# Optimization experiments

Measured on AMD Instinct MI355X. Metric: run time of the kernel, lower is better.

## Reference

```python
import jax, jax.numpy as jnp
import numpy as np

BETA = 0.95
NUM_STEPS = 32


def setup_inputs() -> dict:
    key = jax.random.key(0)
    ks = jax.random.split(key, 6)
    B, IN, D, P = 1024, 512, 256, 8
    total = D * P
    x = jax.random.normal(ks[0], (B, IN), jnp.float32)
    W_proj = jax.random.normal(ks[1], (IN, total), jnp.float32) / np.sqrt(IN)
    b_proj = jnp.zeros((total,), jnp.float32)
    # uniform threshold distribution, sorted: linspace(0.5, 2.0, P)
    thresholds = jnp.linspace(0.5, 2.0, P, dtype=jnp.float32)
    rate_W = jax.random.normal(ks[2], (P, 1), jnp.float32) / np.sqrt(P)
    rate_b = jnp.zeros((1,), jnp.float32)
    conv1_w = jax.random.normal(ks[3], (P // 2, P, 3), jnp.float32) / np.sqrt(P * 3)
    conv1_b = jnp.zeros((P // 2,), jnp.float32)
    conv2_w = jax.random.normal(ks[4], (1, P // 2, 1), jnp.float32) / np.sqrt(P // 2)
    conv2_b = jnp.zeros((1,), jnp.float32)
    fusion = jnp.array([0.6, 0.4], jnp.float32)
    return dict(x=x, W_proj=W_proj, b_proj=b_proj, thresholds=thresholds,
                rate_W=rate_W, rate_b=rate_b, conv1_w=conv1_w, conv1_b=conv1_b,
                conv2_w=conv2_w, conv2_b=conv2_b, fusion=fusion)


def _conv1d(x, w, b):
    # x: [N, C_in, T], w: [C_out, C_in, K] -> [N, C_out, T] (SAME padding)
    y = jax.lax.conv_general_dilated(x, w, window_strides=(1,), padding='SAME',
                                     dimension_numbers=('NCH', 'OIH', 'NCH'))
    return y + b[None, :, None]


def reference(x, W_proj, b_proj, thresholds, rate_W, rate_b,
              conv1_w, conv1_b, conv2_w, conv2_b, fusion):
    B = x.shape[0]
    P = thresholds.shape[0]
    D = W_proj.shape[1] // P
    # constant input current per neuron: [B, D, P]
    I = (x @ W_proj + b_proj).reshape(B, D, P)

    # LIF recurrence (snntorch Leaky, reset_mechanism='subtract'):
    #   reset = H(mem_prev - thr); mem = beta*mem_prev + I - reset*thr; spk = H(mem - thr)
    def step(mem, _):
        reset = (mem > thresholds).astype(mem.dtype)
        mem = BETA * mem + I - reset * thresholds
        spk = (mem > thresholds).astype(mem.dtype)
        return mem, spk

    mem0 = jnp.zeros((B, D, P), x.dtype)
    _, spikes = jax.lax.scan(step, mem0, None, length=NUM_STEPS)  # [T, B, D, P]

    # rate branch
    rates = spikes.mean(axis=0)                        # [B, D, P]
    rate_dec = (rates @ rate_W)[..., 0] + rate_b[0]    # [B, D]

    # temporal branch: [B*D, P, T]
    s = jnp.transpose(spikes, (1, 2, 3, 0)).reshape(B * D, P, NUM_STEPS)
    h = jax.nn.relu(_conv1d(s, conv1_w, conv1_b))
    h = _conv1d(h, conv2_w, conv2_b)                   # [B*D, 1, T]
    temp_dec = h.mean(axis=-1).reshape(B, D)

    fw = jax.nn.softmax(fusion)
    return fw[0] * rate_dec + fw[1] * temp_dec
```

## Files before the change

### kernel.cpp

```cpp
#include <hip/hip_runtime.h>
#include <type_traits>


constexpr int IN_DIM  = 512;
constexpr int D_DIM   = 256;
constexpr int NTOT    = 2048;
constexpr int T_STEPS = 32;

typedef _Float16 f16x8 __attribute__((ext_vector_type(8)));
typedef float    f32x4 __attribute__((ext_vector_type(4)));
typedef ushort   ushort8 __attribute__((ext_vector_type(8)));

#define GLOBAL_AS __attribute__((address_space(1)))
#define LDS_AS    __attribute__((address_space(3)))

__device__ __forceinline__ void split_f16(float v, ushort& h, ushort& l) {
    const _Float16 hf = (_Float16)v;
    const _Float16 lf = (_Float16)((v - (float)hf) * 2048.0f);
    h = __builtin_bit_cast(ushort, hf);
    l = __builtin_bit_cast(ushort, lf);
}

__global__ __launch_bounds__(256)
void popcode_prep(const float* __restrict__ x, const float* __restrict__ Wp,
                  ushort* __restrict__ Ah, ushort* __restrict__ Al,
                  ushort* __restrict__ Bh, ushort* __restrict__ Bl)
{
    __shared__ float tile[64][68];
    const int t = threadIdx.x;
    if (blockIdx.x < 256) {
        const int idx = (blockIdx.x * 256 + t) * 8;
        float v[8];
        *reinterpret_cast<float4*>(v)     = *reinterpret_cast<const float4*>(x + idx);
        *reinterpret_cast<float4*>(v + 4) = *reinterpret_cast<const float4*>(x + idx + 4);
        __align__(16) ushort h[8], l[8];
#pragma unroll
        for (int j = 0; j < 8; ++j) split_f16(v[j], h[j], l[j]);
        *reinterpret_cast<ushort8*>(Ah + idx) = *reinterpret_cast<const ushort8*>(h);
        *reinterpret_cast<ushort8*>(Al + idx) = *reinterpret_cast<const ushort8*>(l);
    } else {
        const int ib = blockIdx.x - 256;
        const int k0 = (ib >> 5) * 64;
        const int c0 = (ib & 31) * 64;
        {
            const int r = t >> 2, cq = (t & 3) * 16;
#pragma unroll
            for (int j = 0; j < 4; ++j)
                *reinterpret_cast<float4*>(&tile[r][cq + j * 4]) =
                    *reinterpret_cast<const float4*>(Wp + (size_t)(k0 + r) * NTOT + c0 + cq + j * 4);
        }
        __syncthreads();
        const int c = t & 63, kq = (t >> 6) * 16;
        __align__(16) ushort h[16], l[16];
#pragma unroll
        for (int j = 0; j < 16; ++j) split_f16(tile[kq + j][c], h[j], l[j]);
        ushort* dh = Bh + (size_t)(c0 + c) * 512 + k0 + kq;
        ushort* dl = Bl + (size_t)(c0 + c) * 512 + k0 + kq;
        *reinterpret_cast<ushort8*>(dh)     = *reinterpret_cast<const ushort8*>(h);
        *reinterpret_cast<ushort8*>(dh + 8) = *reinterpret_cast<const ushort8*>(h + 8);
        *reinterpret_cast<ushort8*>(dl)     = *reinterpret_cast<const ushort8*>(l);
        *reinterpret_cast<ushort8*>(dl + 8) = *reinterpret_cast<const ushort8*>(l + 8);
    }
}

__global__ __launch_bounds__(256, 2)
void popcode_mfma(const ushort* __restrict__ Ah_g, const ushort* __restrict__ Al_g,
                  const ushort* __restrict__ Bh_g, const ushort* __restrict__ Bl_g,
                  float* __restrict__ Iout)
{
    __shared__ __align__(16) ushort Lds[2][4][64][32];

    const int tid  = threadIdx.x;
    const int w    = tid >> 6;
    const int lane = tid & 63;
    const int b0   = blockIdx.x * 64;
    const int c0   = blockIdx.y * 64;

    const ushort* gbase = (w == 0) ? Ah_g : (w == 1) ? Al_g : (w == 2) ? Bh_g : Bl_g;
    const int     t0    = (w < 2) ? b0 : c0;
    const int     srow  = lane >> 2;
    const int     schk  = (lane & 3) * 8;

    const int wr = (w >> 1) * 32;
    const int wc = (w & 1) * 32;
    const int lr = lane & 15;
    const int lg = lane >> 4;

    const f32x4 zero = {0.f, 0.f, 0.f, 0.f};
    f32x4 acch[2][2] = {{zero, zero}, {zero, zero}};
    f32x4 accl[2][2] = {{zero, zero}, {zero, zero}};

    LDS_AS char* lds0 = (LDS_AS char*)&Lds[0][0][0][0];

    auto stage = [&](int buf, int kt) {
        const int koff = kt * 32 + schk;
#pragma unroll
        for (int i = 0; i < 4; ++i) {
            const ushort* src = gbase + (size_t)(t0 + srow + 16 * i) * 512 + koff;
            const int loff = __builtin_amdgcn_readfirstlane(buf * 16384 + w * 4096 + i * 1024);
            __builtin_amdgcn_global_load_lds((const GLOBAL_AS uint*)src,
                                             (LDS_AS uint*)(lds0 + loff), 16, 0, 0);
        }
    };

    auto compute = [&](int buf) {
        f16x8 ah[2], al[2], bh[2], bl[2];
#pragma unroll
        for (int m = 0; m < 2; ++m) {
            const int row = wr + m * 16 + lr;
            ah[m] = *(const f16x8*)&Lds[buf][0][row][lg * 8];
            al[m] = *(const f16x8*)&Lds[buf][1][row][lg * 8];
        }
#pragma unroll
        for (int n = 0; n < 2; ++n) {
            const int col = wc + n * 16 + lr;
            bh[n] = *(const f16x8*)&Lds[buf][2][col][lg * 8];
            bl[n] = *(const f16x8*)&Lds[buf][3][col][lg * 8];
        }
#pragma unroll
        for (int m = 0; m < 2; ++m)
#pragma unroll
            for (int n = 0; n < 2; ++n) {
                acch[m][n] = __builtin_amdgcn_mfma_f32_16x16x32_f16(ah[m], bh[n], acch[m][n], 0, 0, 0);
                accl[m][n] = __builtin_amdgcn_mfma_f32_16x16x32_f16(al[m], bh[n], accl[m][n], 0, 0, 0);
                accl[m][n] = __builtin_amdgcn_mfma_f32_16x16x32_f16(ah[m], bl[n], accl[m][n], 0, 0, 0);
            }
    };

    stage(0, 0);
    __syncthreads();
    for (int kt = 0; kt < 16; ++kt) {
        if (kt < 15) stage((kt + 1) & 1, kt + 1);
        compute(kt & 1);
        __syncthreads();
    }

    const float s = 1.0f / 2048.0f;
#pragma unroll
    for (int m = 0; m < 2; ++m)
#pragma unroll
        for (int n = 0; n < 2; ++n) {
            float* dst = Iout + (size_t)(b0 + wr + m * 16 + lg * 4) * NTOT
                              + c0 + wc + n * 16 + lr;
#pragma unroll
            for (int v = 0; v < 4; ++v)
                dst[(size_t)v * NTOT] = acch[m][n][v] + accl[m][n][v] * s;
        }
}

__global__ __launch_bounds__(256)
void popcode_epi(const float* __restrict__ Iin,
                 const float* __restrict__ bp,
                 const float* __restrict__ thrs,
                 const float* __restrict__ rateW,
                 const float* __restrict__ rateB,
                 const float* __restrict__ c1w,
                 const float* __restrict__ c1b,
                 const float* __restrict__ c2w,
                 const float* __restrict__ c2b,
                 const float* __restrict__ fus,
                 float* __restrict__ out)
{
    __shared__ float lut[3][256][4];
    __shared__ float rlut[256];
    __shared__ float wlds[96];
    __shared__ uint4 exch[256];

    const int tid = threadIdx.x;
    const int wv  = tid >> 6;
    const int h   = wv & 1;
    const int nl  = ((wv >> 1) << 6) | (tid & 63);
    const int n   = blockIdx.x * 128 + nl;
    const int b   = n >> 8;
    const int d   = n & 255;

    if (tid < 96) wlds[tid] = c1w[tid];
    {
        float rv = 0.f;
#pragma unroll
        for (int p = 0; p < 8; ++p)
            rv += (float)((tid >> p) & 1) * rateW[p];
        rlut[tid] = rv;
    }
    __syncthreads();
#pragma unroll
    for (int i = 0; i < 12; ++i) {
        const int e    = 256 * i + tid;
        const int k    = e >> 10;
        const int byte = (e >> 2) & 255;
        const int c    = e & 3;
        float v = (k == 1) ? c1b[c] : 0.f;
#pragma unroll
        for (int p = 0; p < 8; ++p)
            v = fmaf((float)((byte >> p) & 1), wlds[(c * 8 + p) * 3 + k], v);
        (&lut[0][0][0])[e] = v;
    }

    float w2c[4];
#pragma unroll
    for (int c = 0; c < 4; ++c) w2c[c] = c2w[c];
    const float rb_ = rateB[0];
    const float bb2 = c2b[0];
    const float f0 = fus[0], f1 = fus[1];
    const float fm = fmaxf(f0, f1);
    const float e0 = __expf(f0 - fm), e1 = __expf(f1 - fm);
    const float inv = 1.f / (e0 + e1);
    const float fw0 = e0 * inv, fw1 = e1 * inv;

    const size_t base = (size_t)b * NTOT + d * 8 + h * 4;
    const float4 iv   = *reinterpret_cast<const float4*>(Iin + base);
    const float4 bpv  = *reinterpret_cast<const float4*>(bp + d * 8 + h * 4);
    const float4 tv   = *reinterpret_cast<const float4*>(thrs + h * 4);
    float Iv[4]  = {iv.x + bpv.x, iv.y + bpv.y, iv.z + bpv.z, iv.w + bpv.w};
    float thr[4] = {tv.x, tv.y, tv.z, tv.w};
    float Imt[4], mem[4];
    bool  spk[4];
#pragma unroll
    for (int p = 0; p < 4; ++p) {
        Imt[p] = Iv[p] - thr[p];
        mem[p] = 0.f;
        spk[p] = false;
    }

    unsigned nib[4] = {0u, 0u, 0u, 0u};
#pragma unroll
    for (int t = 0; t < T_STEPS; ++t) {
        unsigned nb = 0u;
#pragma unroll
        for (int p = 0; p < 4; ++p) {
            mem[p] = 0.95f * mem[p] + (spk[p] ? Imt[p] : Iv[p]);
            spk[p] = mem[p] > thr[p];
            nb |= spk[p] ? (1u << p) : 0u;
        }
        nib[t >> 3] |= nb << (4 * (t & 7));
    }

    __syncthreads();
    exch[tid] = uint4{nib[0], nib[1], nib[2], nib[3]};
    __syncthreads();
    const uint4 pr = exch[tid ^ 64];
    const unsigned prn[4] = {pr.x, pr.y, pr.z, pr.w};
    unsigned lo[4], hi[4];
#pragma unroll
    for (int w = 0; w < 4; ++w) {
        lo[w] = h ? prn[w] : nib[w];
        hi[w] = h ? nib[w] : prn[w];
    }

    auto getbyte = [&](int t) -> unsigned {
        const int w = t >> 3, s = 4 * (t & 7);
        return ((lo[w] >> s) & 15u) | (((hi[w] >> s) & 15u) << 4);
    };
    const float* lutf = &lut[0][0][0];
    float tacc = 0.f, rsum = 0.f;

    auto conv_half = [&](auto T0C) {
        constexpr int T0 = T0C.value;
        unsigned bprev = (T0 == 0) ? 0u : getbyte(T0 - 1);
        unsigned bcur  = getbyte(T0);
#pragma unroll
        for (int i = 0; i < 16; ++i) {
            const int t = T0 + i;
            const unsigned bnext = (t < 31) ? getbyte(t + 1) : 0u;
            const float4 fa = *reinterpret_cast<const float4*>(lutf + bprev * 4);
            const float4 fb = *reinterpret_cast<const float4*>(lutf + 1024 + bcur * 4);
            const float4 fc = *reinterpret_cast<const float4*>(lutf + 2048 + bnext * 4);
            rsum += rlut[bcur];
            const float h0_ = (fa.x + fb.x) + fc.x;
            const float h1_ = (fa.y + fb.y) + fc.y;
            const float h2_ = (fa.z + fb.z) + fc.z;
            const float h3_ = (fa.w + fb.w) + fc.w;
            tacc = fmaf(fmaxf(h0_, 0.f), w2c[0], tacc);
            tacc = fmaf(fmaxf(h1_, 0.f), w2c[1], tacc);
            tacc = fmaf(fmaxf(h2_, 0.f), w2c[2], tacc);
            tacc = fmaf(fmaxf(h3_, 0.f), w2c[3], tacc);
            bprev = bcur;
            bcur  = bnext;
        }
    };
    if (h == 0) conv_half(std::integral_constant<int, 0>{});
    else        conv_half(std::integral_constant<int, 16>{});

    __syncthreads();
    float2* e2 = reinterpret_cast<float2*>(exch);
    e2[tid] = float2{rsum, tacc};
    __syncthreads();
    const float2 q = e2[tid ^ 64];
    rsum += q.x;
    tacc += q.y;

    if (h == 0) {
        const float rdec = rsum * (1.f / 32.f) + rb_;
        const float temp = tacc * (1.f / 32.f) + bb2;
        out[b * D_DIM + d] = fw0 * rdec + fw1 * temp;
    }
}

extern "C" void kernel_launch(void* const* d_in, const int* in_sizes, int n_in,
                              void* d_out, int out_size, void* d_ws, size_t ws_size,
                              hipStream_t stream) {
    const float* x     = (const float*)d_in[0];
    const float* Wp    = (const float*)d_in[1];
    const float* bp    = (const float*)d_in[2];
    const float* thrs  = (const float*)d_in[3];
    const float* rateW = (const float*)d_in[4];
    const float* rateB = (const float*)d_in[5];
    const float* c1w   = (const float*)d_in[6];
    const float* c1b   = (const float*)d_in[7];
    const float* c2w   = (const float*)d_in[8];
    const float* c2b   = (const float*)d_in[9];
    const float* fus   = (const float*)d_in[10];
    float* out = (float*)d_out;
    float* ws  = (float*)d_ws;

    ushort* Ah = reinterpret_cast<ushort*>(ws);
    ushort* Al = Ah + 1024 * 512;
    ushort* Bh = Al + 1024 * 512;
    ushort* Bl = Bh + 2048 * 512;
    float*  I  = ws + 1536 * 1024;

    popcode_prep<<<dim3(512), dim3(256), 0, stream>>>(x, Wp, Ah, Al, Bh, Bl);
    popcode_mfma<<<dim3(16, 32), dim3(256), 0, stream>>>(Ah, Al, Bh, Bl, I);
    popcode_epi<<<dim3(2048), dim3(256), 0, stream>>>(
        I, bp, thrs, rateW, rateB, c1w, c1b, c2w, c2b, fus, out);
}
```

Measured before the change: 109.0 us.

## Split epilogue conv LUT into nibble tables, popcount rates, remap GEMM blocks per XCD

The epilogue's 256-entry byte LUTs for conv1 are replaced by 16-entry nibble tables, one per half of the 8 populations. This cuts LUT construction work and LDS footprint but doubles the lookups per time step. The rate branch now uses popcount on the spike bitmasks with per-population weights instead of an LDS rate LUT. The MFMA GEMM launches as a 1D grid with a block-index swizzle that groups tiles per XCD for better L2 locality.

Measured after the change: 110.1 us. About the same (+1.0%).

```diff
diff --git a/kernel.cpp b/kernel.cpp
--- a/kernel.cpp
+++ b/kernel.cpp
@@ -73,8 +73,10 @@
     const int tid  = threadIdx.x;
     const int w    = tid >> 6;
     const int lane = tid & 63;
-    const int b0   = blockIdx.x * 64;
-    const int c0   = blockIdx.y * 64;
+
+    const int wg = (blockIdx.x & 7) * 64 + (blockIdx.x >> 3);
+    const int b0 = (wg & 15) * 64;
+    const int c0 = (wg >> 4) * 64;
 
     const ushort* gbase = (w == 0) ? Ah_g : (w == 1) ? Al_g : (w == 2) ? Bh_g : Bl_g;
     const int     t0    = (w < 2) ? b0 : c0;
@@ -161,8 +163,7 @@
                  const float* __restrict__ fus,
                  float* __restrict__ out)
 {
-    __shared__ float lut[3][256][4];
-    __shared__ float rlut[256];
+    __shared__ float lut[3][2][16][4];
     __shared__ float wlds[96];
     __shared__ uint4 exch[256];
 
@@ -175,30 +176,25 @@
     const int d   = n & 255;
 
     if (tid < 96) wlds[tid] = c1w[tid];
-    {
-        float rv = 0.f;
-#pragma unroll
-        for (int p = 0; p < 8; ++p)
-            rv += (float)((tid >> p) & 1) * rateW[p];
-        rlut[tid] = rv;
-    }
-    __syncthreads();
-#pragma unroll
-    for (int i = 0; i < 12; ++i) {
-        const int e    = 256 * i + tid;
-        const int k    = e >> 10;
-        const int byte = (e >> 2) & 255;
-        const int c    = e & 3;
-        float v = (k == 1) ? c1b[c] : 0.f;
-#pragma unroll
-        for (int p = 0; p < 8; ++p)
-            v = fmaf((float)((byte >> p) & 1), wlds[(c * 8 + p) * 3 + k], v);
-        (&lut[0][0][0])[e] = v;
+    __syncthreads();
+    for (int e = tid; e < 384; e += 256) {
+        const int k  = e >> 7;
+        const int j  = (e >> 6) & 1;
+        const int nb = (e >> 2) & 15;
+        const int c  = e & 3;
+        float v = (k == 1 && j == 0) ? c1b[c] : 0.f;
+#pragma unroll
+        for (int p = 0; p < 4; ++p)
+            v = fmaf((float)((nb >> p) & 1), wlds[(c * 8 + j * 4 + p) * 3 + k], v);
+        (&lut[0][0][0][0])[e] = v;
     }
 
     float w2c[4];
 #pragma unroll
     for (int c = 0; c < 4; ++c) w2c[c] = c2w[c];
+    float rW[4];
+#pragma unroll
+    for (int p = 0; p < 4; ++p) rW[p] = rateW[h * 4 + p];
     const float rb_ = rateB[0];
     const float bb2 = c2b[0];
     const float f0 = fus[0], f1 = fus[1];
@@ -235,6 +231,15 @@
         nib[t >> 3] |= nb << (4 * (t & 7));
     }
 
+    float rsum = 0.f;
+#pragma unroll
+    for (int p = 0; p < 4; ++p) {
+        const unsigned m = 0x11111111u << p;
+        const int cnt = __popc(nib[0] & m) + __popc(nib[1] & m)
+                      + __popc(nib[2] & m) + __popc(nib[3] & m);
+        rsum = fmaf((float)cnt, rW[p], rsum);
+    }
+
     __syncthreads();
     exch[tid] = uint4{nib[0], nib[1], nib[2], nib[3]};
     __syncthreads();
@@ -247,35 +252,38 @@
         hi[w] = h ? nib[w] : prn[w];
     }
 
-    auto getbyte = [&](int t) -> unsigned {
-        const int w = t >> 3, s = 4 * (t & 7);
-        return ((lo[w] >> s) & 15u) | (((hi[w] >> s) & 15u) << 4);
+    auto getn = [&](int t, const unsigned* a) -> unsigned {
+        return (a[t >> 3] >> (4 * (t & 7))) & 15u;
     };
-    const float* lutf = &lut[0][0][0];
-    float tacc = 0.f, rsum = 0.f;
+    const float* lutf = &lut[0][0][0][0];
+    float tacc = 0.f;
 
     auto conv_half = [&](auto T0C) {
         constexpr int T0 = T0C.value;
-        unsigned bprev = (T0 == 0) ? 0u : getbyte(T0 - 1);
-        unsigned bcur  = getbyte(T0);
+        unsigned nlp = (T0 == 0) ? 0u : getn(T0 - 1, lo);
+        unsigned nhp = (T0 == 0) ? 0u : getn(T0 - 1, hi);
+        unsigned nlc = getn(T0, lo);
+        unsigned nhc = getn(T0, hi);
 #pragma unroll
         for (int i = 0; i < 16; ++i) {
             const int t = T0 + i;
-            const unsigned bnext = (t < 31) ? getbyte(t + 1) : 0u;
-            const float4 fa = *reinterpret_cast<const float4*>(lutf + bprev * 4);
-            const float4 fb = *reinterpret_cast<const float4*>(lutf + 1024 + bcur * 4);
-            const float4 fc = *reinterpret_cast<const float4*>(lutf + 2048 + bnext * 4);
-            rsum += rlut[bcur];
-            const float h0_ = (fa.x + fb.x) + fc.x;
-            const float h1_ = (fa.y + fb.y) + fc.y;
-            const float h2_ = (fa.z + fb.z) + fc.z;
-            const float h3_ = (fa.w + fb.w) + fc.w;
+            const unsigned nln = (t < 31) ? getn(t + 1, lo) : 0u;
+            const unsigned nhn = (t < 31) ? getn(t + 1, hi) : 0u;
+            const float4 a0 = *reinterpret_cast<const float4*>(lutf + (nlp     ) * 4);
+            const float4 a1 = *reinterpret_cast<const float4*>(lutf + (nhp + 16) * 4);
+            const float4 b0 = *reinterpret_cast<const float4*>(lutf + (nlc + 32) * 4);
+            const float4 b1 = *reinterpret_cast<const float4*>(lutf + (nhc + 48) * 4);
+            const float4 c0 = *reinterpret_cast<const float4*>(lutf + (nln + 64) * 4);
+            const float4 c1 = *reinterpret_cast<const float4*>(lutf + (nhn + 80) * 4);
+            const float h0_ = ((a0.x + a1.x) + (b0.x + b1.x)) + (c0.x + c1.x);
+            const float h1_ = ((a0.y + a1.y) + (b0.y + b1.y)) + (c0.y + c1.y);
+            const float h2_ = ((a0.z + a1.z) + (b0.z + b1.z)) + (c0.z + c1.z);
+            const float h3_ = ((a0.w + a1.w) + (b0.w + b1.w)) + (c0.w + c1.w);
             tacc = fmaf(fmaxf(h0_, 0.f), w2c[0], tacc);
             tacc = fmaf(fmaxf(h1_, 0.f), w2c[1], tacc);
             tacc = fmaf(fmaxf(h2_, 0.f), w2c[2], tacc);
             tacc = fmaf(fmaxf(h3_, 0.f), w2c[3], tacc);
-            bprev = bcur;
-            bcur  = bnext;
+            nlp = nlc; nhp = nhc; nlc = nln; nhc = nhn;
         }
     };
     if (h == 0) conv_half(std::integral_constant<int, 0>{});
@@ -320,7 +328,7 @@
     float*  I  = ws + 1536 * 1024;
 
     popcode_prep<<<dim3(512), dim3(256), 0, stream>>>(x, Wp, Ah, Al, Bh, Bl);
-    popcode_mfma<<<dim3(16, 32), dim3(256), 0, stream>>>(Ah, Al, Bh, Bl, I);
+    popcode_mfma<<<dim3(512), dim3(256), 0, stream>>>(Ah, Al, Bh, Bl, I);
     popcode_epi<<<dim3(2048), dim3(256), 0, stream>>>(
         I, bp, thrs, rateW, rateB, c1w, c1b, c2w, c2b, fus, out);
 }
```
